# Kernel tuning notes

Measured on AMD Instinct MI355X. Metric: run time of the kernel, lower is better.

## Reference

```python
import jax, jax.numpy as jnp
import numpy as np

B, S, D, H = 2, 2048, 1024, 16
HW = D // H  # head width = 64
MASK_FILL = -100000000.0


def setup_inputs() -> dict:
    key0 = jax.random.key(0)
    ks = jax.random.split(key0, 12)
    inp = {
        "query": jax.random.normal(ks[0], (B, S, D), jnp.float32),
        "key": jax.random.normal(ks[1], (B, S, D), jnp.float32),
        "value": jax.random.normal(ks[2], (B, S, D), jnp.float32),
        # bool mask, True masks; broadcasts over batch and heads
        "mask": jax.random.randint(ks[3], (S, S), 0, 2).astype(jnp.bool_),
        # per-head projection kernels: (heads, head_width, d_in)
        "Wq": jax.random.normal(ks[4], (H, HW, D), jnp.float32) * 0.02,
        "bq": jnp.zeros((H, HW), jnp.float32),
        "Wk": jax.random.normal(ks[5], (H, HW, D), jnp.float32) * 0.02,
        "bk": jnp.zeros((H, HW), jnp.float32),
        "Wv": jax.random.normal(ks[6], (H, HW, D), jnp.float32) * 0.02,
        "bv": jnp.zeros((H, HW), jnp.float32),
        # collapse projector: contracts (heads, head_width) -> d_output
        "Wo": jax.random.normal(ks[7], (D, H, HW), jnp.float32) * 0.02,
        "bo": jnp.zeros((D,), jnp.float32),
    }
    return inp


def reference(query, key, value, mask, Wq, bq, Wk, bk, Wv, bv, Wo, bo):
    # head projections -> (b, h, s, w)
    q = jnp.einsum("bsd,hwd->bhsw", query, Wq) + bq[:, None, :]
    k = jnp.einsum("btd,hwd->bhtw", key, Wk) + bk[:, None, :]
    v = jnp.einsum("btd,hwd->bhtw", value, Wv) + bv[:, None, :]
    # unscaled logits, masked_fill, softmax (matches original exactly)
    logits = jnp.einsum("bhsw,bhtw->bhst", q, k)
    logits = jnp.where(mask, MASK_FILL, logits)
    score = jax.nn.softmax(logits, axis=-1)
    # NOTE: original divides AV output by sqrt(head_width) AFTER softmax
    attn = jnp.einsum("bhst,bhtw->bhsw", score, v) / jnp.sqrt(jnp.float32(HW))
    # collapse heads -> (b, s, d_output)
    out = jnp.einsum("bhsw,ohw->bso", attn, Wo) + bo
    return out
```

## Files before the change

### kernel.cpp

```cpp
#include <hip/hip_runtime.h>
#include <hip/hip_bf16.h>
#include <math.h>

#define S_LEN   2048
#define D_MODEL 1024
#define N_HEADS 16
#define HEAD_W  64
#define BATCH   2
#define MROWS   (BATCH * S_LEN)
#define MASK_FILL -100000000.0f
#define LOG2E 1.4426950408889634f

typedef __attribute__((ext_vector_type(8))) short bf16x8;
typedef __attribute__((ext_vector_type(4))) float f32x4;
typedef unsigned short u16;
typedef unsigned int   u32;
typedef unsigned long long u64;

__device__ __forceinline__ float fast_exp2(float x) {
#if __has_builtin(__builtin_amdgcn_exp2f)
    return __builtin_amdgcn_exp2f(x);
#else
    return __builtin_exp2f(x);
#endif
}

__device__ __forceinline__ float fast_rcp(float x) {
#if __has_builtin(__builtin_amdgcn_rcpf)
    return __builtin_amdgcn_rcpf(x);
#else
    return 1.0f / x;
#endif
}

__device__ __forceinline__ u16 f2bf(float f) {
    u32 u = __float_as_uint(f);
    return (u16)((u + 0x7fffu + ((u >> 16) & 1u)) >> 16);
}

__device__ __forceinline__ u32 pack_bf16x2(float lo, float hi) {
    __hip_bfloat162 t = __float22bfloat162_rn(make_float2(lo, hi));
    u32 r;
    __builtin_memcpy(&r, &t, 4);
    return r;
}

__device__ __forceinline__ void gld_lds16(const void* gp, void* lp) {
    __builtin_amdgcn_global_load_lds(
        (const __attribute__((address_space(1))) u32*)gp,
        (__attribute__((address_space(3))) u32*)lp, 16, 0, 0);
}

__device__ __forceinline__ float maskz(float p, u64 w) {
    float r;
    asm("v_cndmask_b32 %0, %1, 0, %2" : "=v"(r) : "v"(p), "s"(w));
    return r;
}

struct CvtJobs {
    const float* src[7];
    u16* dst[7];
    int n[7];
};
__global__ __launch_bounds__(256) void prep_kernel(
    CvtJobs j, const unsigned char* __restrict__ mask, u64* __restrict__ bits) {
    const int t = blockIdx.y;
    if (t < 7) {
        const float* s = j.src[t];
        u16* d = j.dst[t];
        const int n = j.n[t];
        int i = (blockIdx.x * 256 + threadIdx.x) * 4;
        if (i < n) {
            float4 v = *(const float4*)(s + i);
            ushort4 o;
            o.x = f2bf(v.x); o.y = f2bf(v.y); o.z = f2bf(v.z); o.w = f2bf(v.w);
            *(ushort4*)(d + i) = o;
        }
        return;
    }
    if (blockIdx.x >= 2048) return;
    __shared__ int isByte;
    if (threadIdx.x == 0) isByte = 0;
    __syncthreads();
    const int e0 = blockIdx.x * 2048;
    const uint2 v = ((const uint2*)(mask + e0))[threadIdx.x];
    if (((v.x | v.y) & 0xFFFFFF00u) != 0u) isByte = 1;
    __syncthreads();
    const int ib = isByte;
    const int* mi = (const int*)mask;
#pragma unroll
    for (int jj = 0; jj < 8; ++jj) {
        const int e = e0 + jj * 256 + threadIdx.x;
        const bool m = ib ? (mask[e] != 0) : (mi[e] != 0);
        const u64 bl = __ballot(m);
        if ((e & 63) == 0) bits[e >> 6] = bl;
    }
}

__global__ __launch_bounds__(256) void maskt_kernel(
    const u64* __restrict__ bits, u64* __restrict__ words) {
    const int tid = threadIdx.x, wv = tid >> 6, ln = tid & 63;
    const int lane16 = ln & 15, quad = ln >> 4;
    const int sg = blockIdx.x;
#pragma unroll
    for (int ci = 0; ci < 8; ++ci) {
        const int c = wv * 8 + ci;
        const u64 rw = bits[(size_t)(sg * 16 + lane16) * 32 + c];
        u64 keep = 0;
#pragma unroll
        for (int k = 0; k < 16; ++k) {
            const int ntT = k >> 2, r = k & 3;
            const bool m = ((rw >> (ntT * 16 + quad * 4 + r)) & 1ull) != 0ull;
            const u64 bl = __ballot(m);
            if (ln == k) keep = bl;
        }
        if (ln < 16) words[(((size_t)sg * 32 + c) << 4) + ln] = keep;
    }
}

__device__ __forceinline__ void gemm_core_bf16(const u16* __restrict__ A,
                                               const u16* __restrict__ Bt,
                                               int m0, int n0, f32x4 acc[4][4]) {
    __shared__ u16 As[2][4096];
    __shared__ u16 Bs[2][4096];
    const int tid = threadIdx.x;
    const int wv = tid >> 6, ln = tid & 63;
    const int lane16 = ln & 15, quad = ln >> 4;
    const int wr = (wv >> 1) * 64, wc = (wv & 1) * 64;
    const u16* A0 = A + (size_t)(m0 + ln) * D_MODEL + wv * 8;
    const u16* A1 = A + (size_t)(m0 + 64 + ln) * D_MODEL + wv * 8;
    const u16* B0 = Bt + (size_t)(n0 + ln) * D_MODEL + wv * 8;
    const u16* B1 = Bt + (size_t)(n0 + 64 + ln) * D_MODEL + wv * 8;

    gld_lds16(A0, &As[0][wv * 1024]);
    gld_lds16(A1, &As[0][wv * 1024 + 512]);
    gld_lds16(B0, &Bs[0][wv * 1024]);
    gld_lds16(B1, &Bs[0][wv * 1024 + 512]);

    for (int kt = 0; kt < D_MODEL / 32; ++kt) {
        const int buf = kt & 1;
        __syncthreads();
        if (kt < D_MODEL / 32 - 1) {
            const int ko = (kt + 1) * 32;
            gld_lds16(A0 + ko, &As[buf ^ 1][wv * 1024]);
            gld_lds16(A1 + ko, &As[buf ^ 1][wv * 1024 + 512]);
            gld_lds16(B0 + ko, &Bs[buf ^ 1][wv * 1024]);
            gld_lds16(B1 + ko, &Bs[buf ^ 1][wv * 1024 + 512]);
        }
        bf16x8 af[4], bfv[4];
#pragma unroll
        for (int mt = 0; mt < 4; ++mt)
            af[mt] = *(const bf16x8*)&As[buf][quad * 1024 + (wr + mt * 16 + lane16) * 8];
#pragma unroll
        for (int nt = 0; nt < 4; ++nt)
            bfv[nt] = *(const bf16x8*)&Bs[buf][quad * 1024 + (wc + nt * 16 + lane16) * 8];
#pragma unroll
        for (int mt = 0; mt < 4; ++mt)
#pragma unroll
            for (int nt = 0; nt < 4; ++nt)
                acc[mt][nt] = __builtin_amdgcn_mfma_f32_16x16x32_bf16(
                    af[mt], bfv[nt], acc[mt][nt], 0, 0, 0);
    }
}

__global__ __launch_bounds__(256, 4) void qkv_gemm_kernel(
    const u16* __restrict__ xq, const u16* __restrict__ xk, const u16* __restrict__ xv,
    const u16* __restrict__ wq, const u16* __restrict__ wk, const u16* __restrict__ wv,
    const float* __restrict__ bq, const float* __restrict__ bk, const float* __restrict__ bv,
    u16* __restrict__ qb, u16* __restrict__ kb, u16* __restrict__ vtmp) {
    const u16* A; const u16* Bt; const float* bias; u16* outp;
    const int z = blockIdx.z;
    if (z == 0)      { A = xq; Bt = wq; bias = bq; outp = qb; }
    else if (z == 1) { A = xk; Bt = wk; bias = bk; outp = kb; }
    else             { A = xv; Bt = wv; bias = bv; outp = vtmp; }
    f32x4 acc[4][4] = {};
    const int m0 = blockIdx.y * 128, n0 = blockIdx.x * 128;
    gemm_core_bf16(A, Bt, m0, n0, acc);

    const int tid = threadIdx.x;
    const int wvi = tid >> 6, ln = tid & 63;
    const int lane16 = ln & 15, quad = ln >> 4;
    const int wr = (wvi >> 1) * 64, wc = (wvi & 1) * 64;
    const float scale = (z == 0) ? LOG2E : 1.0f;
#pragma unroll
    for (int nt = 0; nt < 4; ++nt) {
        const int n = n0 + wc + nt * 16 + lane16;
        const float bb = bias[n];
        const int h = n >> 6, w = n & 63;
#pragma unroll
        for (int mt = 0; mt < 4; ++mt)
#pragma unroll
            for (int r = 0; r < 4; ++r) {
                const int m = m0 + wr + mt * 16 + quad * 4 + r;
                const int bidx = m >> 11, s = m & 2047;
                outp[((size_t)((bidx * N_HEADS + h) * S_LEN + s)) * HEAD_W + w] =
                    f2bf((acc[mt][nt][r] + bb) * scale);
            }
    }
}

__global__ __launch_bounds__(256) void vtrans_kernel(
    const u16* __restrict__ vtmp, u16* __restrict__ vbt) {
    __shared__ u16 T[64][72];
    const int tid = threadIdx.x;
    const int bh = blockIdx.y;
    const int s0 = blockIdx.x * 64;
    const int row = tid >> 2, seg = (tid & 3) * 16;
    const u16* src = vtmp + ((size_t)bh * S_LEN + s0 + row) * HEAD_W + seg;
    uint4 a = *(const uint4*)src;
    uint4 b2 = *(const uint4*)(src + 8);
    u16 tmp[16];
    *(uint4*)tmp = a; *(uint4*)(tmp + 8) = b2;
#pragma unroll
    for (int j = 0; j < 16; ++j) T[seg + j][row] = tmp[j];
    __syncthreads();
    u16* dst = vbt + ((size_t)bh * HEAD_W + row) * S_LEN + s0 + seg;
    *(uint4*)dst       = *(const uint4*)&T[row][seg];
    *(uint4*)(dst + 8) = *(const uint4*)&T[row][seg + 8];
}

__global__ __launch_bounds__(256, 4) void out_gemm_kernel(
    const u16* __restrict__ ab, const u16* __restrict__ wo,
    const float* __restrict__ bo, float* __restrict__ out) {
    f32x4 acc[4][4] = {};
    const int m0 = blockIdx.y * 128, n0 = blockIdx.x * 128;
    gemm_core_bf16(ab, wo, m0, n0, acc);
    const int tid = threadIdx.x;
    const int wvi = tid >> 6, ln = tid & 63;
    const int lane16 = ln & 15, quad = ln >> 4;
    const int wr = (wvi >> 1) * 64, wc = (wvi & 1) * 64;
#pragma unroll
    for (int nt = 0; nt < 4; ++nt) {
        const int n = n0 + wc + nt * 16 + lane16;
        const float bb = bo[n];
#pragma unroll
        for (int mt = 0; mt < 4; ++mt)
#pragma unroll
            for (int r = 0; r < 4; ++r) {
                const int m = m0 + wr + mt * 16 + quad * 4 + r;
                out[(size_t)m * D_MODEL + n] = acc[mt][nt][r] + bb;
            }
    }
}

__global__ __launch_bounds__(256, 3) void attn_kernel(
    const u16* __restrict__ qbuf, const u16* __restrict__ kbuf,
    const u16* __restrict__ vbt, const u64* __restrict__ maskw,
    float* __restrict__ Opart, float* __restrict__ lpart) {
    __shared__ u16 Ks[2][4096];
    __shared__ u16 Vt[2][4096];
    __shared__ u16 Ps[4][32 * 72];
    const int tid = threadIdx.x;
    const int wv = tid >> 6, ln = tid & 63;
    const int lane16 = ln & 15, quad = ln >> 4;
    const int fid = (blockIdx.z * N_HEADS + blockIdx.y) * (S_LEN / 128) + blockIdx.x;
    const int nid = (fid & 7) * 128 + (fid >> 3);
    const int s_blk = (nid & 15) * 128;
    const int rest = nid >> 4;
    const int h = rest & 15;
    const int bz = rest >> 4;
    const int b = bz >> 1, hf = bz & 1;
    const int c0 = hf * 16;
    const size_t hb = ((size_t)(b * N_HEADS + h)) * S_LEN * HEAD_W;
    const u16* Qg = qbuf + hb;
    const u16* Kg = kbuf + hb;
    const u16* Vg = vbt + hb;
    const int sg0 = (s_blk >> 4) + wv * 2;

    bf16x8 qa[2][2];
#pragma unroll
    for (int mt = 0; mt < 2; ++mt)
#pragma unroll
        for (int kk = 0; kk < 2; ++kk)
            qa[mt][kk] = *(const bf16x8*)(Qg +
                (size_t)(s_blk + wv * 32 + mt * 16 + lane16) * HEAD_W + kk * 32 + quad * 8);

    {
        const int t0g = c0 * 64;
        const int i0 = 2 * wv, i1 = 2 * wv + 1;
        gld_lds16(Kg + (size_t)(t0g + ln) * HEAD_W + i0 * 8, &Ks[0][i0 * 512]);
        gld_lds16(Kg + (size_t)(t0g + ln) * HEAD_W + i1 * 8, &Ks[0][i1 * 512]);
        gld_lds16(Vg + (size_t)ln * S_LEN + t0g + i0 * 8, &Vt[0][i0 * 512]);
        gld_lds16(Vg + (size_t)ln * S_LEN + t0g + i1 * 8, &Vt[0][i1 * 512]);
    }

    bf16x8 ones;
#pragma unroll
    for (int i = 0; i < 8; ++i) ones[i] = (short)0x3F80;

    f32x4 oacc[2][4] = {};
    f32x4 lacc[2] = {};

    for (int ci = 0; ci < 16; ++ci) {
        const int c = c0 + ci;
        const int buf = ci & 1;
        __syncthreads();
        if (ci < 15) {
            const int t1 = (c + 1) * 64;
            const int i0 = 2 * wv, i1 = 2 * wv + 1;
            gld_lds16(Kg + (size_t)(t1 + ln) * HEAD_W + i0 * 8, &Ks[buf ^ 1][i0 * 512]);
            gld_lds16(Kg + (size_t)(t1 + ln) * HEAD_W + i1 * 8, &Ks[buf ^ 1][i1 * 512]);
            gld_lds16(Vg + (size_t)ln * S_LEN + t1 + i0 * 8, &Vt[buf ^ 1][i0 * 512]);
            gld_lds16(Vg + (size_t)ln * S_LEN + t1 + i1 * 8, &Vt[buf ^ 1][i1 * 512]);
        }

        f32x4 st[4][2] = {};
#pragma unroll
        for (int kk = 0; kk < 2; ++kk)
#pragma unroll
            for (int ntT = 0; ntT < 4; ++ntT) {
                bf16x8 kf = *(const bf16x8*)&Ks[buf][(kk * 4 + quad) * 512 + (ntT * 16 + lane16) * 8];
#pragma unroll
                for (int mt = 0; mt < 2; ++mt)
                    st[ntT][mt] = __builtin_amdgcn_mfma_f32_16x16x32_bf16(
                        kf, qa[mt][kk], st[ntT][mt], 0, 0, 0);
            }

#pragma unroll
        for (int mt = 0; mt < 2; ++mt) {
            const u64* __restrict__ wp = maskw +
                __builtin_amdgcn_readfirstlane((((sg0 + mt) * 32 + c) << 4));
#pragma unroll
            for (int ntT = 0; ntT < 4; ++ntT) {
                const float p0 = maskz(fast_exp2(st[ntT][mt][0]), wp[ntT * 4 + 0]);
                const float p1 = maskz(fast_exp2(st[ntT][mt][1]), wp[ntT * 4 + 1]);
                const float p2 = maskz(fast_exp2(st[ntT][mt][2]), wp[ntT * 4 + 2]);
                const float p3 = maskz(fast_exp2(st[ntT][mt][3]), wp[ntT * 4 + 3]);
                uint2 pk;
                pk.x = pack_bf16x2(p0, p1);
                pk.y = pack_bf16x2(p2, p3);
                *(uint2*)&Ps[wv][(mt * 16 + lane16) * 72 + ntT * 16 + quad * 4] = pk;
            }
        }

        bf16x8 pf[2][2];
#pragma unroll
        for (int mt = 0; mt < 2; ++mt)
#pragma unroll
            for (int kk = 0; kk < 2; ++kk)
                pf[mt][kk] = *(const bf16x8*)&Ps[wv][(mt * 16 + lane16) * 72 + kk * 32 + quad * 8];
#pragma unroll
        for (int kk = 0; kk < 2; ++kk) {
#pragma unroll
            for (int mt = 0; mt < 2; ++mt)
                lacc[mt] = __builtin_amdgcn_mfma_f32_16x16x32_bf16(
                    pf[mt][kk], ones, lacc[mt], 0, 0, 0);
#pragma unroll
            for (int ntw = 0; ntw < 4; ++ntw) {
                bf16x8 vf = *(const bf16x8*)&Vt[buf][(kk * 4 + quad) * 512 + (ntw * 16 + lane16) * 8];
#pragma unroll
                for (int mt = 0; mt < 2; ++mt)
                    oacc[mt][ntw] = __builtin_amdgcn_mfma_f32_16x16x32_bf16(
                        pf[mt][kk], vf, oacc[mt][ntw], 0, 0, 0);
            }
        }
    }

    float* OpB = Opart + ((size_t)(hf * 4096 + b * 2048)) * 1024;
#pragma unroll
    for (int mt = 0; mt < 2; ++mt) {
#pragma unroll
        for (int r = 0; r < 4; ++r) {
            const int s = s_blk + wv * 32 + mt * 16 + quad * 4 + r;
            float* dst = OpB + (size_t)s * 1024 + h * 64;
#pragma unroll
            for (int ntw = 0; ntw < 4; ++ntw)
                dst[ntw * 16 + lane16] = oacc[mt][ntw][r];
        }
        if (lane16 == 0) {
#pragma unroll
            for (int r = 0; r < 4; ++r) {
                const int srow = s_blk + wv * 32 + mt * 16 + quad * 4 + r;
                lpart[(size_t)(hf * 4096 + b * 2048 + srow) * 16 + h] = lacc[mt][r];
            }
        }
    }
}

__global__ __launch_bounds__(256) void combine_kernel(
    const float* __restrict__ Op, const float* __restrict__ lp,
    u16* __restrict__ ab) {
    const int idx4 = blockIdx.x * 256 + threadIdx.x;
    const int row = idx4 >> 8;
    const int d = (idx4 & 255) * 4;
    const int h = d >> 6;
    const float l = lp[(size_t)row * 16 + h] + lp[(size_t)(4096 + row) * 16 + h];
    const float inv = 0.125f * fast_rcp(l);
    float4 a = *(const float4*)(Op + (size_t)row * 1024 + d);
    float4 b = *(const float4*)(Op + (size_t)(4096 + row) * 1024 + d);
    ushort4 o;
    o.x = f2bf((a.x + b.x) * inv);
    o.y = f2bf((a.y + b.y) * inv);
    o.z = f2bf((a.z + b.z) * inv);
    o.w = f2bf((a.w + b.w) * inv);
    *(ushort4*)(ab + (size_t)row * 1024 + d) = o;
}

extern "C" void kernel_launch(void* const* d_in, const int* in_sizes, int n_in,
                              void* d_out, int out_size, void* d_ws, size_t ws_size,
                              hipStream_t stream) {
    const float* query = (const float*)d_in[0];
    const float* key   = (const float*)d_in[1];
    const float* value = (const float*)d_in[2];
    const void*  mask  = d_in[3];
    const float* Wq = (const float*)d_in[4];
    const float* bq = (const float*)d_in[5];
    const float* Wk = (const float*)d_in[6];
    const float* bk = (const float*)d_in[7];
    const float* Wv = (const float*)d_in[8];
    const float* bv = (const float*)d_in[9];
    const float* Wo = (const float*)d_in[10];
    const float* bo = (const float*)d_in[11];
    float* out = (float*)d_out;

    char* ws = (char*)d_ws;
    const size_t MB = 1024 * 1024;
    u64* bits  = (u64*)ws;
    u64* maskt = (u64*)(ws + 512 * 1024);
    u16* wob  = (u16*)(ws + 1 * MB);
    u16* qb   = (u16*)(ws + 3 * MB);
    u16* kb   = (u16*)(ws + 11 * MB);
    u16* vbt  = (u16*)(ws + 19 * MB);
    char* uA = ws + 27 * MB;
    u16* xq   = (u16*)(uA);
    u16* xk   = (u16*)(uA + 8 * MB);
    u16* xv   = (u16*)(uA + 16 * MB);
    u16* wqb  = (u16*)(uA + 24 * MB);
    u16* wkb  = (u16*)(uA + 26 * MB);
    u16* wvb  = (u16*)(uA + 28 * MB);
    u16* vtmp = (u16*)(uA + 30 * MB);
    float* Opart = (float*)(uA);
    float* lpart = (float*)(uA + 32 * MB);
    u16* ab = qb;

    const size_t NACT = (size_t)MROWS * D_MODEL;
    const size_t NW   = (size_t)D_MODEL * D_MODEL;

    CvtJobs j;
    j.src[0] = query; j.dst[0] = xq;  j.n[0] = (int)NACT;
    j.src[1] = key;   j.dst[1] = xk;  j.n[1] = (int)NACT;
    j.src[2] = value; j.dst[2] = xv;  j.n[2] = (int)NACT;
    j.src[3] = Wq;    j.dst[3] = wqb; j.n[3] = (int)NW;
    j.src[4] = Wk;    j.dst[4] = wkb; j.n[4] = (int)NW;
    j.src[5] = Wv;    j.dst[5] = wvb; j.n[5] = (int)NW;
    j.src[6] = Wo;    j.dst[6] = wob; j.n[6] = (int)NW;
    prep_kernel<<<dim3(NACT / 1024, 8), 256, 0, stream>>>(
        j, (const unsigned char*)mask, bits);
    maskt_kernel<<<dim3(128), 256, 0, stream>>>(bits, maskt);

    qkv_gemm_kernel<<<dim3(D_MODEL / 128, MROWS / 128, 3), 256, 0, stream>>>(
        xq, xk, xv, wqb, wkb, wvb, bq, bk, bv, qb, kb, vtmp);
    vtrans_kernel<<<dim3(S_LEN / 64, BATCH * N_HEADS), 256, 0, stream>>>(vtmp, vbt);
    attn_kernel<<<dim3(S_LEN / 128, N_HEADS, BATCH * 2), 256, 0, stream>>>(
        qb, kb, vbt, maskt, Opart, lpart);
    combine_kernel<<<4096, 256, 0, stream>>>(Opart, lpart, ab);
    out_gemm_kernel<<<dim3(D_MODEL / 128, MROWS / 128), 256, 0, stream>>>(
        ab, wob, bo, out);
}
```

Baseline: 302.5 us.

## Switch attention MFMAs to 32x32x16 tiles and compute row sums in registers

The attention kernel now uses 32x32x16 bf16 MFMA instructions in place of 16x16x32, and the Q fragments, score layout, P staging, output store and mask-word layout all change to match the 32x32 output format. The mask transpose kernel is rewritten for the new 32-row word layout. The row-sum MFMA against a ones vector is replaced by a per-lane register accumulation of the fp32 probabilities plus a cross-half shuffle. This aims to cut the number of MFMA issues and the LDS fragment reads per tile. The catch is a different register footprint under a launch bound of 3 blocks per CU, and row sums now taken in fp32 instead of from bf16-rounded values.

```diff
diff --git a/kernel.cpp b/kernel.cpp
--- a/kernel.cpp
+++ b/kernel.cpp
@@ -13,6 +13,7 @@
 
 typedef __attribute__((ext_vector_type(8))) short bf16x8;
 typedef __attribute__((ext_vector_type(4))) float f32x4;
+typedef __attribute__((ext_vector_type(16))) float f32x16;
 typedef unsigned short u16;
 typedef unsigned int   u32;
 typedef unsigned long long u64;
@@ -100,21 +101,21 @@
 __global__ __launch_bounds__(256) void maskt_kernel(
     const u64* __restrict__ bits, u64* __restrict__ words) {
     const int tid = threadIdx.x, wv = tid >> 6, ln = tid & 63;
-    const int lane16 = ln & 15, quad = ln >> 4;
+    const int l31 = ln & 31, hi = ln >> 5;
     const int sg = blockIdx.x;
 #pragma unroll
     for (int ci = 0; ci < 8; ++ci) {
         const int c = wv * 8 + ci;
-        const u64 rw = bits[(size_t)(sg * 16 + lane16) * 32 + c];
+        const u64 rw = bits[(size_t)(sg * 32 + l31) * 32 + c];
         u64 keep = 0;
 #pragma unroll
-        for (int k = 0; k < 16; ++k) {
-            const int ntT = k >> 2, r = k & 3;
-            const bool m = ((rw >> (ntT * 16 + quad * 4 + r)) & 1ull) != 0ull;
+        for (int k = 0; k < 32; ++k) {
+            const int T = k >> 4, g = (k >> 2) & 3, q = k & 3;
+            const bool m = ((rw >> (T * 32 + q + 8 * g + 4 * hi)) & 1ull) != 0ull;
             const u64 bl = __ballot(m);
             if (ln == k) keep = bl;
         }
-        if (ln < 16) words[(((size_t)sg * 32 + c) << 4) + ln] = keep;
+        if (ln < 32) words[((size_t)(sg * 32 + c) << 5) + ln] = keep;
     }
 }
 
@@ -252,7 +253,7 @@
     __shared__ u16 Ps[4][32 * 72];
     const int tid = threadIdx.x;
     const int wv = tid >> 6, ln = tid & 63;
-    const int lane16 = ln & 15, quad = ln >> 4;
+    const int l31 = ln & 31, hi = ln >> 5;
     const int fid = (blockIdx.z * N_HEADS + blockIdx.y) * (S_LEN / 128) + blockIdx.x;
     const int nid = (fid & 7) * 128 + (fid >> 3);
     const int s_blk = (nid & 15) * 128;
@@ -265,15 +266,13 @@
     const u16* Qg = qbuf + hb;
     const u16* Kg = kbuf + hb;
     const u16* Vg = vbt + hb;
-    const int sg0 = (s_blk >> 4) + wv * 2;
-
-    bf16x8 qa[2][2];
-#pragma unroll
-    for (int mt = 0; mt < 2; ++mt)
-#pragma unroll
-        for (int kk = 0; kk < 2; ++kk)
-            qa[mt][kk] = *(const bf16x8*)(Qg +
-                (size_t)(s_blk + wv * 32 + mt * 16 + lane16) * HEAD_W + kk * 32 + quad * 8);
+    const int sgw = (s_blk >> 5) + wv;
+
+    bf16x8 qa2[4];
+#pragma unroll
+    for (int ks = 0; ks < 4; ++ks)
+        qa2[ks] = *(const bf16x8*)(Qg +
+            (size_t)(s_blk + wv * 32 + l31) * HEAD_W + ks * 16 + hi * 8);
 
     {
         const int t0g = c0 * 64;
@@ -284,12 +283,8 @@
         gld_lds16(Vg + (size_t)ln * S_LEN + t0g + i1 * 8, &Vt[0][i1 * 512]);
     }
 
-    bf16x8 ones;
-#pragma unroll
-    for (int i = 0; i < 8; ++i) ones[i] = (short)0x3F80;
-
-    f32x4 oacc[2][4] = {};
-    f32x4 lacc[2] = {};
+    f32x16 oacc2[2] = {};
+    float lsum = 0.0f;
 
     for (int ci = 0; ci < 16; ++ci) {
         const int c = c0 + ci;
@@ -304,76 +299,60 @@
             gld_lds16(Vg + (size_t)ln * S_LEN + t1 + i1 * 8, &Vt[buf ^ 1][i1 * 512]);
         }
 
-        f32x4 st[4][2] = {};
-#pragma unroll
-        for (int kk = 0; kk < 2; ++kk)
-#pragma unroll
-            for (int ntT = 0; ntT < 4; ++ntT) {
-                bf16x8 kf = *(const bf16x8*)&Ks[buf][(kk * 4 + quad) * 512 + (ntT * 16 + lane16) * 8];
-#pragma unroll
-                for (int mt = 0; mt < 2; ++mt)
-                    st[ntT][mt] = __builtin_amdgcn_mfma_f32_16x16x32_bf16(
-                        kf, qa[mt][kk], st[ntT][mt], 0, 0, 0);
+#pragma unroll
+        for (int T = 0; T < 2; ++T) {
+            f32x16 st = {};
+#pragma unroll
+            for (int ks = 0; ks < 4; ++ks) {
+                const bf16x8 kf = *(const bf16x8*)&Ks[buf][
+                    (ks * 2 + hi) * 512 + (T * 32 + l31) * 8];
+                st = __builtin_amdgcn_mfma_f32_32x32x16_bf16(
+                    kf, qa2[ks], st, 0, 0, 0);
             }
-
-#pragma unroll
-        for (int mt = 0; mt < 2; ++mt) {
             const u64* __restrict__ wp = maskw +
-                __builtin_amdgcn_readfirstlane((((sg0 + mt) * 32 + c) << 4));
-#pragma unroll
-            for (int ntT = 0; ntT < 4; ++ntT) {
-                const float p0 = maskz(fast_exp2(st[ntT][mt][0]), wp[ntT * 4 + 0]);
-                const float p1 = maskz(fast_exp2(st[ntT][mt][1]), wp[ntT * 4 + 1]);
-                const float p2 = maskz(fast_exp2(st[ntT][mt][2]), wp[ntT * 4 + 2]);
-                const float p3 = maskz(fast_exp2(st[ntT][mt][3]), wp[ntT * 4 + 3]);
+                __builtin_amdgcn_readfirstlane(((sgw * 32 + c) << 5) + T * 16);
+#pragma unroll
+            for (int g = 0; g < 4; ++g) {
+                const float p0 = maskz(fast_exp2(st[4 * g + 0]), wp[4 * g + 0]);
+                const float p1 = maskz(fast_exp2(st[4 * g + 1]), wp[4 * g + 1]);
+                const float p2 = maskz(fast_exp2(st[4 * g + 2]), wp[4 * g + 2]);
+                const float p3 = maskz(fast_exp2(st[4 * g + 3]), wp[4 * g + 3]);
+                lsum += (p0 + p1) + (p2 + p3);
                 uint2 pk;
                 pk.x = pack_bf16x2(p0, p1);
                 pk.y = pack_bf16x2(p2, p3);
-                *(uint2*)&Ps[wv][(mt * 16 + lane16) * 72 + ntT * 16 + quad * 4] = pk;
+                *(uint2*)&Ps[wv][l31 * 72 + T * 32 + 8 * g + 4 * hi] = pk;
             }
         }
 
-        bf16x8 pf[2][2];
-#pragma unroll
-        for (int mt = 0; mt < 2; ++mt)
-#pragma unroll
-            for (int kk = 0; kk < 2; ++kk)
-                pf[mt][kk] = *(const bf16x8*)&Ps[wv][(mt * 16 + lane16) * 72 + kk * 32 + quad * 8];
-#pragma unroll
-        for (int kk = 0; kk < 2; ++kk) {
-#pragma unroll
-            for (int mt = 0; mt < 2; ++mt)
-                lacc[mt] = __builtin_amdgcn_mfma_f32_16x16x32_bf16(
-                    pf[mt][kk], ones, lacc[mt], 0, 0, 0);
-#pragma unroll
-            for (int ntw = 0; ntw < 4; ++ntw) {
-                bf16x8 vf = *(const bf16x8*)&Vt[buf][(kk * 4 + quad) * 512 + (ntw * 16 + lane16) * 8];
-#pragma unroll
-                for (int mt = 0; mt < 2; ++mt)
-                    oacc[mt][ntw] = __builtin_amdgcn_mfma_f32_16x16x32_bf16(
-                        pf[mt][kk], vf, oacc[mt][ntw], 0, 0, 0);
+#pragma unroll
+        for (int T = 0; T < 2; ++T)
+#pragma unroll
+            for (int gg = 0; gg < 2; ++gg) {
+                const bf16x8 pf = *(const bf16x8*)&Ps[wv][
+                    l31 * 72 + T * 32 + gg * 16 + hi * 8];
+#pragma unroll
+                for (int W = 0; W < 2; ++W) {
+                    const bf16x8 vf = *(const bf16x8*)&Vt[buf][
+                        (T * 4 + gg * 2 + hi) * 512 + (W * 32 + l31) * 8];
+                    oacc2[W] = __builtin_amdgcn_mfma_f32_32x32x16_bf16(
+                        pf, vf, oacc2[W], 0, 0, 0);
+                }
             }
-        }
     }
 
     float* OpB = Opart + ((size_t)(hf * 4096 + b * 2048)) * 1024;
 #pragma unroll
-    for (int mt = 0; mt < 2; ++mt) {
-#pragma unroll
-        for (int r = 0; r < 4; ++r) {
-            const int s = s_blk + wv * 32 + mt * 16 + quad * 4 + r;
-            float* dst = OpB + (size_t)s * 1024 + h * 64;
-#pragma unroll
-            for (int ntw = 0; ntw < 4; ++ntw)
-                dst[ntw * 16 + lane16] = oacc[mt][ntw][r];
-        }
-        if (lane16 == 0) {
-#pragma unroll
-            for (int r = 0; r < 4; ++r) {
-                const int srow = s_blk + wv * 32 + mt * 16 + quad * 4 + r;
-                lpart[(size_t)(hf * 4096 + b * 2048 + srow) * 16 + h] = lacc[mt][r];
-            }
-        }
+    for (int W = 0; W < 2; ++W)
+#pragma unroll
+        for (int r = 0; r < 16; ++r) {
+            const int s = s_blk + wv * 32 + (r & 3) + 8 * (r >> 2) + 4 * hi;
+            OpB[(size_t)s * 1024 + h * 64 + W * 32 + l31] = oacc2[W][r];
+        }
+    lsum += __shfl_xor(lsum, 32);
+    if (ln < 32) {
+        const int srow = s_blk + wv * 32 + ln;
+        lpart[(size_t)(hf * 4096 + b * 2048 + srow) * 16 + h] = lsum;
     }
 }
 
@@ -446,7 +425,7 @@
     j.src[6] = Wo;    j.dst[6] = wob; j.n[6] = (int)NW;
     prep_kernel<<<dim3(NACT / 1024, 8), 256, 0, stream>>>(
         j, (const unsigned char*)mask, bits);
-    maskt_kernel<<<dim3(128), 256, 0, stream>>>(bits, maskt);
+    maskt_kernel<<<dim3(64), 256, 0, stream>>>(bits, maskt);
 
     qkv_gemm_kernel<<<dim3(D_MODEL / 128, MROWS / 128, 3), 256, 0, stream>>>(
         xq, xk, xv, wqb, wkb, wvb, bq, bk, bv, qb, kb, vtmp);
```

Result: slower. 312.5 us (+3.3%).
